# Performance work log

Measured on AMD Instinct MI355X. Metric: run time of the kernel, lower is better.

## Reference

```python
import jax, jax.numpy as jnp
import numpy as np

B, N, NC = 16, 128, 32          # batch, num_vectors, num_condition_vectors
H, A, DEG = 256, 64, 3          # hidden_dim, attention_dim, degree
SCALE = float(np.sqrt(H) ** DEG)  # weights_scale = sqrt(hidden_dim)^degree = 4096
# S3 non-identity permutations lifted to batch tensor axes (batch axis 0 fixed)
PERMS = [(0, 1, 3, 2), (0, 2, 1, 3), (0, 2, 3, 1), (0, 3, 1, 2), (0, 3, 2, 1)]


def setup_inputs() -> dict:
    key = jax.random.key(0)
    ks = jax.random.split(key, 6)
    inv = 1.0 / np.sqrt(H)
    return {
        "x": jax.random.normal(ks[0], (B, N, H), jnp.float32),
        "x_mask": jnp.ones((B, N, 1), jnp.float32),
        "condition": jax.random.normal(ks[1], (B, NC, H), jnp.float32),
        "condition_mask": jnp.ones((B, NC, 1), jnp.float32),
        "W1": (jax.random.normal(ks[2], (DEG, H, H), jnp.float32) * inv),
        "b1": jnp.zeros((DEG, H), jnp.float32),
        "Wc": (jax.random.normal(ks[3], (DEG, H, H), jnp.float32) * inv),
        "Wlin": (jax.random.normal(ks[4], (DEG, H, A), jnp.float32) * inv),
        "blin": jnp.zeros((DEG, A), jnp.float32),
    }


def reference(x, x_mask, condition, condition_mask, W1, b1, Wc, Wlin, blin):
    # masked mean-pool of condition vectors: [B, H]
    pooled = (condition * condition_mask).sum(1) / jnp.maximum(condition_mask.sum(1), 1.0)
    ys, dvs = [], []
    for d in range(DEG):  # small fixed loop over structurally distinct branches
        dv = pooled @ Wc[d]                                   # daughter vector [B, H]
        h = jax.nn.gelu(x @ W1[d] + b1[d] + dv[:, None, :])   # branch encoder [B, N, H]
        y = (h @ Wlin[d] + blin[d]) * x_mask                  # linear + mask  [B, N, A]
        ys.append(y)
        dvs.append(dv)
    # degree-3 multilinear contraction: 'xbi,ybi,zbi->bxyz' == 'bxi,byi,bzi->bxyz'
    base = jnp.einsum('bxi,byi,bzi->bxyz', ys[0], ys[1], ys[2]) / SCALE
    # symmetrize: add all non-identity permuted views (S3 minus identity)
    out = base
    for p in PERMS:
        out = out + jnp.transpose(base, p)
    return out, jnp.stack(dvs)  # ([B,N,N,N], [DEG,B,H])
```

## Files before the change

### kernel.cpp

```cpp
#include <hip/hip_runtime.h>
#include <hip/hip_bf16.h>
#include <math.h>
#include <string.h>

#define BB   16
#define NN   128
#define NCC  32
#define HH   256
#define AA   64
#define DEGN 3
#define BNR  (BB*NN)

typedef __bf16 bf16x8 __attribute__((ext_vector_type(8)));
typedef float  f32x16 __attribute__((ext_vector_type(16)));

__device__ __forceinline__ unsigned int pk2(float lo, float hi) {
    __hip_bfloat162 h2 = __float22bfloat162_rn(make_float2(lo, hi));
    unsigned int u;
    memcpy(&u, &h2, 4);
    return u;
}
__device__ __forceinline__ unsigned short bfbits(float f) {
    __hip_bfloat16 h = __float2bfloat16(f);
    unsigned short u;
    memcpy(&u, &h, 2);
    return u;
}

__global__ __launch_bounds__(256) void k_head(const float* __restrict__ cond,
                                              const float* __restrict__ cmask,
                                              const float* __restrict__ Wc,
                                              const float* __restrict__ W1,
                                              const float* __restrict__ Wlin,
                                              float* __restrict__ dv,
                                              float* __restrict__ dv_out,
                                              unsigned short* __restrict__ W1t,
                                              unsigned short* __restrict__ Wlt) {
    __shared__ float shm[32 * 33];
    const int bid = blockIdx.x, t = threadIdx.x;

    if (bid < 48) {
        const int d = bid >> 4, b = bid & 15;
        float s = 0.f, ms = 0.f;
        for (int c = 0; c < NCC; ++c) {
            float mk = cmask[b * NCC + c];
            s  += cond[(b * NCC + c) * HH + t] * mk;
            ms += mk;
        }
        shm[t] = s / fmaxf(ms, 1.0f);
        __syncthreads();
        const float* Wd = Wc + (size_t)d * HH * HH;
        float acc = 0.f;
        for (int k = 0; k < HH; ++k) acc += shm[k] * Wd[k * HH + t];
        int idx = (d * BB + b) * HH + t;
        dv[idx]     = acc;
        dv_out[idx] = acc;
    } else if (bid < 240) {
        const int q = bid - 48;
        const int d = q >> 6, r2 = q & 63, tk = r2 >> 3, tn = r2 & 7;
        float (*tile)[33] = (float (*)[33])shm;
        #pragma unroll
        for (int p = 0; p < 4; ++p) {
            int kr = p * 8 + (t >> 5), nr = t & 31;
            tile[kr][nr] = W1[((size_t)d * HH + tk * 32 + kr) * HH + tn * 32 + nr];
        }
        __syncthreads();
        #pragma unroll
        for (int p = 0; p < 4; ++p) {
            int nr = p * 8 + (t >> 5), kr = t & 31;
            W1t[((size_t)d * HH + tn * 32 + nr) * HH + tk * 32 + kr] =
                bfbits(tile[kr][nr]);
        }
    } else {
        const int q = bid - 240;
        const int d = q >> 4, r3 = q & 15, tk = r3 >> 1, ta = r3 & 1;
        float (*tile)[33] = (float (*)[33])shm;
        #pragma unroll
        for (int p = 0; p < 4; ++p) {
            int kr = p * 8 + (t >> 5), ar = t & 31;
            tile[kr][ar] = Wlin[((size_t)d * HH + tk * 32 + kr) * AA + ta * 32 + ar];
        }
        __syncthreads();
        #pragma unroll
        for (int p = 0; p < 4; ++p) {
            int ar = p * 8 + (t >> 5), kr = t & 31;
            Wlt[((size_t)d * AA + ta * 32 + ar) * HH + tk * 32 + kr] =
                bfbits(tile[kr][ar]);
        }
    }
}

__global__ __launch_bounds__(256) void k_mlp(const float* __restrict__ x,
                                             const float* __restrict__ xmask,
                                             const float* __restrict__ b1,
                                             const float* __restrict__ blin,
                                             const float* __restrict__ dv,
                                             const unsigned short* __restrict__ W1t,
                                             const unsigned short* __restrict__ Wlt,
                                             float* __restrict__ yv) {
    __shared__ __align__(16) char ldsA[32 * 512];
    __shared__ float ps[2][32][68];

    const int t = threadIdx.x;
    const int d = blockIdx.x >> 6, rt = blockIdx.x & 63;
    const int row0 = rt * 32;
    const int b = row0 >> 7;
    const int lane = t & 63, wid = t >> 6;
    const int rl5 = lane & 31, h2v = lane >> 5;

    #pragma unroll
    for (int it = 0; it < 8; ++it) {
        const int r = wid * 8 + it;
        const float4 v = *(const float4*)&x[(size_t)(row0 + r) * HH + lane * 4];
        uint2 u = make_uint2(pk2(v.x, v.y), pk2(v.z, v.w));
        *(uint2*)(ldsA + r * 512 + ((lane * 8) ^ ((r & 7) << 4))) = u;
    }
    __syncthreads();

    f32x16 acc1[2];
    #pragma unroll
    for (int nt = 0; nt < 2; ++nt)
        #pragma unroll
        for (int e = 0; e < 16; ++e) acc1[nt][e] = 0.f;

    #pragma unroll
    for (int ks = 0; ks < 16; ++ks) {
        bf16x8 af = *(const bf16x8*)(ldsA + rl5 * 512 +
                      ((ks * 32 + h2v * 16) ^ ((rl5 & 7) << 4)));
        #pragma unroll
        for (int nt = 0; nt < 2; ++nt) {
            const int n = wid * 64 + nt * 32 + rl5;
            bf16x8 bf = *(const bf16x8*)(W1t +
                          ((size_t)d * HH + n) * HH + ks * 16 + h2v * 8);
            acc1[nt] = __builtin_amdgcn_mfma_f32_32x32x16_bf16(af, bf, acc1[nt], 0, 0, 0);
        }
    }
    __syncthreads();

    #pragma unroll
    for (int nt = 0; nt < 2; ++nt) {
        const int col = wid * 64 + nt * 32 + rl5;
        const float add = b1[d * HH + col] + dv[(d * BB + b) * HH + col];
        #pragma unroll
        for (int e = 0; e < 16; ++e) {
            const int row = (e & 3) + 8 * (e >> 2) + 4 * h2v;
            float v = acc1[nt][e] + add;
            float u = 0.7978845608028654f * (v + 0.044715f * v * v * v);
            float g = 0.5f * v * (1.0f + tanhf(u));
            *(unsigned short*)(ldsA + row * 512 + ((col * 2) ^ ((row & 7) << 4))) =
                bfbits(g);
        }
    }
    __syncthreads();

    const int qc = wid >> 1, kh = wid & 1;
    f32x16 acc2;
    #pragma unroll
    for (int e = 0; e < 16; ++e) acc2[e] = 0.f;
    #pragma unroll
    for (int ks = 0; ks < 8; ++ks) {
        const int kk = kh * 8 + ks;
        bf16x8 af = *(const bf16x8*)(ldsA + rl5 * 512 +
                      ((kk * 32 + h2v * 16) ^ ((rl5 & 7) << 4)));
        bf16x8 bf = *(const bf16x8*)(Wlt +
                      ((size_t)d * AA + qc * 32 + rl5) * HH + kk * 16 + h2v * 8);
        acc2 = __builtin_amdgcn_mfma_f32_32x32x16_bf16(af, bf, acc2, 0, 0, 0);
    }
    #pragma unroll
    for (int e = 0; e < 16; ++e) {
        const int row = (e & 3) + 8 * (e >> 2) + 4 * h2v;
        ps[kh][row][qc * 32 + rl5] = acc2[e];
    }
    __syncthreads();

    #pragma unroll
    for (int j = 0; j < 8; ++j) {
        const int idx = t * 8 + j;
        const int row = idx >> 6, a = idx & 63;
        float v = ps[0][row][a] + ps[1][row][a] + blin[d * AA + a];
        v *= xmask[row0 + row];
        yv[((size_t)d * BNR + row0 + row) * AA + a] = v;
    }
}

__device__ __forceinline__ void lds_fence_barrier() {
    asm volatile("s_waitcnt lgkmcnt(0)" ::: "memory");
    __builtin_amdgcn_s_barrier();
    __builtin_amdgcn_sched_barrier(0);
}

#define LROW 128

__global__ __launch_bounds__(256, 2) void k_contract(const float* __restrict__ yv,
                                                     float* __restrict__ outp) {
    __shared__ __align__(16) char lds[4 * 128 * LROW];
    char* A1b = lds;
    char* A2b = lds + 1 * 128 * LROW;
    char* B1b = lds + 2 * 128 * LROW;
    char* B2b = lds + 3 * 128 * LROW;

    const int t  = threadIdx.x;
    const int b  = blockIdx.x >> 5;
    const int xg = blockIdx.x & 31;

    const float* y0p = yv + (size_t)(0 * BNR + b * NN) * AA;
    const float* y1p = yv + (size_t)(1 * BNR + b * NN) * AA;
    const float* y2p = yv + (size_t)(2 * BNR + b * NN) * AA;

    const int lane = t & 63;
    const int wid  = t >> 6;
    const int li   = lane & 31;
    const int rh   = lane >> 5;

    #pragma unroll
    for (int it = 0; it < 16; ++it) {
        const int r   = wid * 32 + it * 2 + rh;
        const int swz = (r & 7) << 4;
        const float2 v1 = *(const float2*)&y1p[r * AA + 2 * li];
        const float2 v2 = *(const float2*)&y2p[r * AA + 2 * li];
        *(unsigned int*)(B1b + r * LROW + ((4 * li) ^ swz)) = pk2(v2.x, v2.y);
        *(unsigned int*)(B2b + r * LROW + ((4 * li) ^ swz)) = pk2(v1.x, v1.y);
    }

    const int wy  = (wid >> 1) * 64, wz = (wid & 1) * 64;
    const int rl5 = lane & 31, h2v = lane >> 5;
    const float inv = 1.0f / 4096.0f;

    for (int xi = 0; xi < 4; ++xi) {
        const int xr = xg * 4 + xi;
        const float s0 = y0p[xr * AA + lane];
        const float s1 = y1p[xr * AA + lane];
        const float s2 = y2p[xr * AA + lane];
        const float s0a = __shfl(s0, 2 * li), s0b = __shfl(s0, 2 * li + 1);
        const float s1a = __shfl(s1, 2 * li), s1b = __shfl(s1, 2 * li + 1);
        const float s2a = __shfl(s2, 2 * li), s2b = __shfl(s2, 2 * li + 1);

        #pragma unroll
        for (int it = 0; it < 16; ++it) {
            const int r   = wid * 32 + it * 2 + rh;
            const int swz = (r & 7) << 4;
            const float2 v0 = *(const float2*)&y0p[r * AA + 2 * li];
            const float2 v1 = *(const float2*)&y1p[r * AA + 2 * li];
            unsigned int a1 = pk2(s0a * v1.x + s1a * v0.x, s0b * v1.y + s1b * v0.y);
            unsigned int a2 = pk2(s2a * v0.x, s2b * v0.y);
            *(unsigned int*)(A1b + r * LROW + ((4 * li) ^ swz)) = a1;
            *(unsigned int*)(A2b + r * LROW + ((4 * li) ^ swz)) = a2;
        }
        lds_fence_barrier();

        f32x16 acc[2][2];
        #pragma unroll
        for (int mi = 0; mi < 2; ++mi)
            #pragma unroll
            for (int ni = 0; ni < 2; ++ni)
                #pragma unroll
                for (int e = 0; e < 16; ++e) acc[mi][ni][e] = 0.f;

        #pragma unroll
        for (int p = 0; p < 4; ++p) {
            const char* Ua = (p == 0) ? A1b : (p == 1) ? B1b : (p == 2) ? A2b : B2b;
            const char* Va = (p == 0) ? B1b : (p == 1) ? A1b : (p == 2) ? B2b : A2b;
            #pragma unroll
            for (int ks = 0; ks < 4; ++ks) {
                bf16x8 af[2], bf[2];
                #pragma unroll
                for (int mi = 0; mi < 2; ++mi) {
                    int row = wy + mi * 32 + rl5;
                    af[mi] = *(const bf16x8*)(Ua + row * LROW +
                              ((ks * 32 + h2v * 16) ^ ((row & 7) << 4)));
                }
                #pragma unroll
                for (int ni = 0; ni < 2; ++ni) {
                    int row = wz + ni * 32 + rl5;
                    bf[ni] = *(const bf16x8*)(Va + row * LROW +
                              ((ks * 32 + h2v * 16) ^ ((row & 7) << 4)));
                }
                #pragma unroll
                for (int mi = 0; mi < 2; ++mi)
                    #pragma unroll
                    for (int ni = 0; ni < 2; ++ni)
                        acc[mi][ni] = __builtin_amdgcn_mfma_f32_32x32x16_bf16(
                            af[mi], bf[ni], acc[mi][ni], 0, 0, 0);
            }
        }
        lds_fence_barrier();

        float* Cs = (float*)lds;
        float* osl = outp + ((size_t)(b * NN + xr)) * (NN * NN);
        #pragma unroll
        for (int ph = 0; ph < 2; ++ph) {
            if ((wid >> 1) == ph) {
                #pragma unroll
                for (int mi = 0; mi < 2; ++mi) {
                    #pragma unroll
                    for (int ni = 0; ni < 2; ++ni) {
                        const int colb = wz + ni * 32 + rl5;
                        #pragma unroll
                        for (int e = 0; e < 16; ++e) {
                            int rowf = (e & 3) + 8 * (e >> 2) + 4 * h2v;
                            Cs[(mi * 32 + rowf) * NN + colb] = acc[mi][ni][e] * inv;
                        }
                    }
                }
            }
            lds_fence_barrier();
            #pragma unroll
            for (int it2 = 0; it2 < 8; ++it2) {
                const int rloc = wid * 16 + it2 * 2 + rh;
                float4 v = *(const float4*)&Cs[rloc * NN + rl5 * 4];
                *(float4*)&osl[(size_t)(ph * 64 + rloc) * NN + rl5 * 4] = v;
            }
            lds_fence_barrier();
        }
    }
}

extern "C" void kernel_launch(void* const* d_in, const int* in_sizes, int n_in,
                              void* d_out, int out_size, void* d_ws, size_t ws_size,
                              hipStream_t stream) {
    const float* x     = (const float*)d_in[0];
    const float* xmask = (const float*)d_in[1];
    const float* cond  = (const float*)d_in[2];
    const float* cmask = (const float*)d_in[3];
    const float* W1    = (const float*)d_in[4];
    const float* b1    = (const float*)d_in[5];
    const float* Wc    = (const float*)d_in[6];
    const float* Wlin  = (const float*)d_in[7];
    const float* blin  = (const float*)d_in[8];

    float* out = (float*)d_out;
    float* ws  = (float*)d_ws;

    float* dv  = ws;
    float* yv  = ws + 12288;
    unsigned short* W1t = (unsigned short*)((char*)d_ws + (size_t)(12288 + 393216) * 4);
    unsigned short* Wlt = W1t + (size_t)DEGN * HH * HH;
    float* dv_out = out + (size_t)BB * NN * NN * NN;

    k_head    <<<dim3(288), dim3(256), 0, stream>>>(cond, cmask, Wc, W1, Wlin,
                                                    dv, dv_out, W1t, Wlt);
    k_mlp     <<<dim3(DEGN * 64), dim3(256), 0, stream>>>(x, xmask, b1, blin, dv,
                                                          W1t, Wlt, yv);
    k_contract<<<dim3(BB * NN / 4), dim3(256), 0, stream>>>(yv, out);
}
```

Before: 57.59 us.

## Retile contraction waves to 32x128 strips with per-wave private epilogue staging

Each wave now owns a 32-row by 128-column output strip instead of a 64x64 quadrant. It loads one A fragment and four B fragments per k-step. The output epilogue stages accumulators through a wave-private slice of the A buffers, so it needs only wave-level LDS waits instead of block-wide barriers. This is meant to remove the four block barriers and the serialized two-phase write-out per x row. The cost is one extra LDS fragment read per four MFMAs, and the code relies on each wave's staging slice matching the A rows it alone writes.

```diff
diff --git a/kernel.cpp b/kernel.cpp
--- a/kernel.cpp
+++ b/kernel.cpp
@@ -188,6 +188,10 @@
     __builtin_amdgcn_s_barrier();
     __builtin_amdgcn_sched_barrier(0);
 }
+__device__ __forceinline__ void lds_wave_wait() {
+    asm volatile("s_waitcnt lgkmcnt(0)" ::: "memory");
+    __builtin_amdgcn_sched_barrier(0);
+}
 
 #define LROW 128
 
@@ -222,18 +226,21 @@
         *(unsigned int*)(B2b + r * LROW + ((4 * li) ^ swz)) = pk2(v1.x, v1.y);
     }
 
-    const int wy  = (wid >> 1) * 64, wz = (wid & 1) * 64;
     const int rl5 = lane & 31, h2v = lane >> 5;
+    const int wy  = wid * 32;
     const float inv = 1.0f / 4096.0f;
+
+    char* s1 = A1b + wid * 4096;
+    char* s2 = A2b + wid * 4096;
 
     for (int xi = 0; xi < 4; ++xi) {
         const int xr = xg * 4 + xi;
         const float s0 = y0p[xr * AA + lane];
-        const float s1 = y1p[xr * AA + lane];
-        const float s2 = y2p[xr * AA + lane];
-        const float s0a = __shfl(s0, 2 * li), s0b = __shfl(s0, 2 * li + 1);
-        const float s1a = __shfl(s1, 2 * li), s1b = __shfl(s1, 2 * li + 1);
-        const float s2a = __shfl(s2, 2 * li), s2b = __shfl(s2, 2 * li + 1);
+        const float s1v = y1p[xr * AA + lane];
+        const float s2v = y2p[xr * AA + lane];
+        const float s0a = __shfl(s0, 2 * li),  s0b = __shfl(s0, 2 * li + 1);
+        const float s1a = __shfl(s1v, 2 * li), s1b = __shfl(s1v, 2 * li + 1);
+        const float s2a = __shfl(s2v, 2 * li), s2b = __shfl(s2v, 2 * li + 1);
 
         #pragma unroll
         for (int it = 0; it < 16; ++it) {
@@ -248,13 +255,11 @@
         }
         lds_fence_barrier();
 
-        f32x16 acc[2][2];
-        #pragma unroll
-        for (int mi = 0; mi < 2; ++mi)
+        f32x16 acc[4];
+        #pragma unroll
+        for (int ni = 0; ni < 4; ++ni)
             #pragma unroll
-            for (int ni = 0; ni < 2; ++ni)
-                #pragma unroll
-                for (int e = 0; e < 16; ++e) acc[mi][ni][e] = 0.f;
+            for (int e = 0; e < 16; ++e) acc[ni][e] = 0.f;
 
         #pragma unroll
         for (int p = 0; p < 4; ++p) {
@@ -262,55 +267,45 @@
             const char* Va = (p == 0) ? B1b : (p == 1) ? A1b : (p == 2) ? B2b : A2b;
             #pragma unroll
             for (int ks = 0; ks < 4; ++ks) {
-                bf16x8 af[2], bf[2];
+                const int arow = wy + rl5;
+                bf16x8 af = *(const bf16x8*)(Ua + arow * LROW +
+                              ((ks * 32 + h2v * 16) ^ ((arow & 7) << 4)));
                 #pragma unroll
-                for (int mi = 0; mi < 2; ++mi) {
-                    int row = wy + mi * 32 + rl5;
-                    af[mi] = *(const bf16x8*)(Ua + row * LROW +
-                              ((ks * 32 + h2v * 16) ^ ((row & 7) << 4)));
-                }
-                #pragma unroll
-                for (int ni = 0; ni < 2; ++ni) {
-                    int row = wz + ni * 32 + rl5;
-                    bf[ni] = *(const bf16x8*)(Va + row * LROW +
-                              ((ks * 32 + h2v * 16) ^ ((row & 7) << 4)));
-                }
-                #pragma unroll
-                for (int mi = 0; mi < 2; ++mi)
-                    #pragma unroll
-                    for (int ni = 0; ni < 2; ++ni)
-                        acc[mi][ni] = __builtin_amdgcn_mfma_f32_32x32x16_bf16(
-                            af[mi], bf[ni], acc[mi][ni], 0, 0, 0);
-            }
-        }
-        lds_fence_barrier();
-
-        float* Cs = (float*)lds;
-        float* osl = outp + ((size_t)(b * NN + xr)) * (NN * NN);
-        #pragma unroll
-        for (int ph = 0; ph < 2; ++ph) {
-            if ((wid >> 1) == ph) {
-                #pragma unroll
-                for (int mi = 0; mi < 2; ++mi) {
-                    #pragma unroll
-                    for (int ni = 0; ni < 2; ++ni) {
-                        const int colb = wz + ni * 32 + rl5;
-                        #pragma unroll
-                        for (int e = 0; e < 16; ++e) {
-                            int rowf = (e & 3) + 8 * (e >> 2) + 4 * h2v;
-                            Cs[(mi * 32 + rowf) * NN + colb] = acc[mi][ni][e] * inv;
-                        }
-                    }
+                for (int ni = 0; ni < 4; ++ni) {
+                    const int brow = ni * 32 + rl5;
+                    bf16x8 bf = *(const bf16x8*)(Va + brow * LROW +
+                                  ((ks * 32 + h2v * 16) ^ ((brow & 7) << 4)));
+                    acc[ni] = __builtin_amdgcn_mfma_f32_32x32x16_bf16(
+                        af, bf, acc[ni], 0, 0, 0);
                 }
             }
-            lds_fence_barrier();
+        }
+        lds_fence_barrier();
+
+        float* osl = outp + ((size_t)(b * NN + xr)) * (NN * NN);
+        #pragma unroll
+        for (int half = 0; half < 2; ++half) {
+            #pragma unroll
+            for (int ni = 0; ni < 4; ++ni) {
+                const int colb = ni * 32 + rl5;
+                #pragma unroll
+                for (int e2 = 0; e2 < 8; ++e2) {
+                    const int e    = half * 8 + e2;
+                    const int rloc = (e2 & 3) + 8 * (e2 >> 2) + 4 * h2v;
+                    char* reg = (e2 < 4) ? s1 : s2;
+                    *(float*)(reg + ((rloc & 7) * 512) + colb * 4) =
+                        acc[ni][e] * inv;
+                }
+            }
+            lds_wave_wait();
             #pragma unroll
             for (int it2 = 0; it2 < 8; ++it2) {
-                const int rloc = wid * 16 + it2 * 2 + rh;
-                float4 v = *(const float4*)&Cs[rloc * NN + rl5 * 4];
-                *(float4*)&osl[(size_t)(ph * 64 + rloc) * NN + rl5 * 4] = v;
+                const int rloc = it2 * 2 + rh;
+                const char* reg = (it2 < 4) ? s1 : s2;
+                float4 v = *(const float4*)(reg + ((rloc & 7) * 512) + rl5 * 16);
+                *(float4*)&osl[(size_t)(wy + half * 16 + rloc) * NN + rl5 * 4] = v;
             }
-            lds_fence_barrier();
+            lds_wave_wait();
         }
     }
 }
```

Result: no change. 57.35 us (-0.4%).
